# Kernel tuning notes

Hardware: AMD Instinct MI355X
Metric: run time of the kernel (lower is better)

Reference implementation:

```python
import jax, jax.numpy as jnp
import numpy as np

NC = 65536   # candidate centers across FPN levels (single image)
NP = 1024    # proposal boxes == points
D = 256      # points_feat_dim
C = 256      # in_channels (query/key dim)
START_LEVEL = 3
NEG = -1e30


def setup_inputs() -> dict:
    key = jax.random.key(0)
    ks = jax.random.split(key, 9)
    # centers: [y, x, size, stride]; stride in {8,16,32,64,128} -> lvl 0..4
    lvl = jax.random.randint(ks[0], (NC,), 0, 5)
    stride = (2.0 ** (lvl + START_LEVEL)).astype(jnp.float32)
    yx = jax.random.uniform(ks[1], (NC, 2), minval=0.0, maxval=1024.0)
    centers = jnp.concatenate([yx, stride[:, None], stride[:, None]], axis=1)
    # boxes: [x1, y1, x2, y2]
    x1y1 = jax.random.uniform(ks[2], (NP, 2), minval=0.0, maxval=900.0)
    wh = jax.random.uniform(ks[3], (NP, 2), minval=64.0, maxval=256.0)
    boxes = jnp.concatenate([x1y1, x1y1 + wh], axis=1)
    points_feat = jax.random.normal(ks[4], (NP, D), dtype=jnp.float32)
    box_feat = jax.random.normal(ks[5], (NC, D), dtype=jnp.float32)
    Wq = jax.random.normal(ks[6], (D, C), dtype=jnp.float32) / np.sqrt(D).astype(np.float32)
    bq = jnp.zeros((C,), dtype=jnp.float32)
    Wk = jax.random.normal(ks[7], (D, C), dtype=jnp.float32) / np.sqrt(D).astype(np.float32)
    bk = jnp.zeros((C,), dtype=jnp.float32)
    scales = 1.0 + 0.1 * jax.random.normal(ks[8], (5,), dtype=jnp.float32)
    return dict(points_feat=points_feat, box_feat=box_feat, centers=centers,
                boxes=boxes, Wq=Wq, bq=bq, Wk=Wk, bk=bk, scales=scales)


def reference(points_feat, box_feat, centers, boxes, Wq, bq, Wk, bk, scales):
    # geometry -> containment mask [NC, NP] (center c inside box p)
    coord = centers[:, :2] + jnp.floor_divide(centers[:, 2:3], 2.0)  # [NC,2]
    ys, xs = coord[:, 0], coord[:, 1]
    l = xs[:, None] - boxes[None, :, 0]
    t = ys[:, None] - boxes[None, :, 1]
    r = boxes[None, :, 2] - xs[:, None]
    b = boxes[None, :, 3] - ys[:, None]
    mask = jnp.minimum(jnp.minimum(l, t), jnp.minimum(r, b)) > 0     # [NC,NP]

    stride = centers[:, 3]
    lvl = (jnp.log2(stride) - START_LEVEL).astype(jnp.int32)         # [NC] in 0..4
    w = scales[lvl]                                                  # per-level scale

    query = points_feat @ Wq + bq                                    # [NP,C]
    keyf = (box_feat * w[:, None]) @ Wk + bk                         # [NC,C]

    sim = jnp.clip(keyf @ query.T, -50.0, 50.0)                      # [NC,NP]
    logits = jnp.where(mask, sim, NEG)
    attn = jax.nn.softmax(logits, axis=0)
    attn = jnp.where(mask, attn, 0.0)                                # zero out invalid
    merge = attn.T @ box_feat                                        # [NP,D]
    return points_feat + merge
```

## Files before the change

kernel.cpp:

```cpp
#include <hip/hip_runtime.h>

typedef unsigned short ushort_t;
typedef _Float16 half8 __attribute__((ext_vector_type(8)));
typedef short short8 __attribute__((ext_vector_type(8)));
typedef float floatx4 __attribute__((ext_vector_type(4)));

#define NCC 65536
#define NPP 1024
#define DD 256
#define NCHUNK 64
#define VROW 36
#define VTILE_B (256 * VROW * 2)
#define L2E 1.44269504f
#define CLIPL 72.134752f

static __device__ __forceinline__ ushort_t f2h_bits(float x) {
  _Float16 h = (_Float16)x;
  return __builtin_bit_cast(ushort_t, h);
}
static __device__ __forceinline__ ushort_t f2bf_bits(float x) {
  unsigned u = __builtin_bit_cast(unsigned, x);
  unsigned r = (u + 0x7FFFu + ((u >> 16) & 1u)) >> 16;
  return (ushort_t)r;
}
static __device__ __forceinline__ float bf2f(ushort_t b) {
  unsigned u = ((unsigned)b) << 16;
  return __builtin_bit_cast(float, u);
}
static __device__ __forceinline__ half8 cvt8(const float* p) {
  float4 a = *(const float4*)p, b = *(const float4*)(p + 4);
  half8 h;
  h[0] = (_Float16)a.x; h[1] = (_Float16)a.y; h[2] = (_Float16)a.z; h[3] = (_Float16)a.w;
  h[4] = (_Float16)b.x; h[5] = (_Float16)b.y; h[6] = (_Float16)b.z; h[7] = (_Float16)b.w;
  return h;
}
static __device__ __forceinline__ void dma16(const void* g, void* l) {
  __builtin_amdgcn_global_load_lds((const __attribute__((address_space(1))) unsigned int*)g,
                                   (__attribute__((address_space(3))) unsigned int*)l, 16, 0, 0);
}
static __device__ __forceinline__ short8 mk_s8(uint2 lo, uint2 hi) {
  uint4 u;
  u.x = lo.x; u.y = lo.y; u.z = hi.x; u.w = hi.y;
  return __builtin_bit_cast(short8, u);
}

__global__ __launch_bounds__(256) void mk_prep(const float* __restrict__ Wq,
                                               const float* __restrict__ Wk,
                                               const float* __restrict__ bq,
                                               const float* __restrict__ bk,
                                               ushort_t* __restrict__ Mk, float* __restrict__ tu,
                                               float* __restrict__ tv, float* __restrict__ s0v) {
  const int t = threadIdx.x;
  if (blockIdx.x == 16) {
    float su = 0.f, sv = 0.f;
    for (int j = 0; j < DD; j += 4) {
      float4 a = *(const float4*)&Wk[(size_t)t * DD + j];
      float4 b = *(const float4*)&bq[j];
      su += a.x * b.x + a.y * b.y + a.z * b.z + a.w * b.w;
      float4 c = *(const float4*)&Wq[(size_t)t * DD + j];
      float4 d = *(const float4*)&bk[j];
      sv += c.x * d.x + c.y * d.y + c.z * d.z + c.w * d.w;
    }
    tu[t] = su;
    tv[t] = sv;
    __shared__ float red[256];
    red[t] = bk[t] * bq[t];
    __syncthreads();
    for (int o = 128; o; o >>= 1) {
      if (t < o) red[t] += red[t + o];
      __syncthreads();
    }
    if (t == 0) s0v[0] = red[0];
    return;
  }
  const int m0 = ((int)blockIdx.x & 3) * 64, e0 = ((int)blockIdx.x >> 2) * 64;
  const int w = t >> 6, lane = t & 63, qd = lane >> 4, n = lane & 15;
  floatx4 acc[4] = {};
#pragma unroll
  for (int s = 0; s < 8; s++) {
    half8 af = cvt8(&Wk[(size_t)(m0 + w * 16 + n) * DD + s * 32 + qd * 8]);
#pragma unroll
    for (int nt = 0; nt < 4; ++nt) {
      half8 bf = cvt8(&Wq[(size_t)(e0 + nt * 16 + n) * DD + s * 32 + qd * 8]);
      acc[nt] = __builtin_amdgcn_mfma_f32_16x16x32_f16(af, bf, acc[nt], 0, 0, 0);
    }
  }
#pragma unroll
  for (int nt = 0; nt < 4; ++nt)
#pragma unroll
    for (int r = 0; r < 4; r++)
      Mk[(size_t)(m0 + w * 16 + qd * 4 + r) * DD + e0 + nt * 16 + n] = f2h_bits(acc[nt][r]);
}

__global__ __launch_bounds__(256) void gt_prep(const float* __restrict__ pf,
                                               const ushort_t* __restrict__ Mk,
                                               const float* __restrict__ tv,
                                               const float* __restrict__ s0v,
                                               ushort_t* __restrict__ Gt,
                                               float* __restrict__ gamma) {
  const int t = threadIdx.x, p0 = (int)blockIdx.x * 64;
  const int w = t >> 6, lane = t & 63, qd = lane >> 4, n = lane & 15;
  floatx4 acc[16] = {};
#pragma unroll
  for (int s = 0; s < 8; s++) {
    half8 af = cvt8(&pf[(size_t)(p0 + w * 16 + n) * DD + s * 32 + qd * 8]);
#pragma unroll
    for (int nt = 0; nt < 16; ++nt) {
      half8 bf = __builtin_bit_cast(half8,
                                    *(const uint4*)&Mk[(size_t)(nt * 16 + n) * DD + s * 32 + qd * 8]);
      acc[nt] = __builtin_amdgcn_mfma_f32_16x16x32_f16(af, bf, acc[nt], 0, 0, 0);
    }
  }
#pragma unroll
  for (int nt = 0; nt < 16; ++nt)
#pragma unroll
    for (int r = 0; r < 4; r++)
      Gt[(size_t)(p0 + w * 16 + qd * 4 + r) * DD + nt * 16 + n] = f2h_bits(acc[nt][r]);
  if (t < 64) {
    float s = s0v[0];
    for (int j = 0; j < DD; j += 4) {
      float4 a = *(const float4*)&pf[(size_t)(p0 + t) * DD + j];
      float4 b = *(const float4*)&tv[j];
      s += a.x * b.x + a.y * b.y + a.z * b.z + a.w * b.w;
    }
    gamma[p0 + t] = s * L2E - CLIPL;
  }
}

__global__ __launch_bounds__(256) void bt_prep(const float* __restrict__ bf,
                                               const float* __restrict__ centers,
                                               const float* __restrict__ scales,
                                               const float* __restrict__ tu,
                                               ushort_t* __restrict__ bfR,
                                               ushort_t* __restrict__ vTb,
                                               float4* __restrict__ meta) {
  __shared__ float tu_s[256];
  __shared__ __align__(16) ushort_t lt[256][40];
  const int t = threadIdx.x, c0 = (int)blockIdx.x * 32;
  tu_s[t] = tu[t];
  __syncthreads();
  const int c = t >> 3, sub = t & 7;
  float du = 0.f;
#pragma unroll
  for (int i = 0; i < 8; i++) {
    int f4 = sub + 8 * i;
    int d0 = f4 * 4;
    float4 v = *(const float4*)&bf[(size_t)(c0 + c) * DD + d0];
    du += v.x * tu_s[d0] + v.y * tu_s[d0 + 1] + v.z * tu_s[d0 + 2] + v.w * tu_s[d0 + 3];
    int l = f4 >> 1;
    int u = (l & ~7) | ((l & 7) ^ (c & 7));
    ushort_t h0 = f2h_bits(v.x), h1 = f2h_bits(v.y), h2 = f2h_bits(v.z), h3 = f2h_bits(v.w);
    *(uint2*)&bfR[(size_t)(c0 + c) * DD + u * 8 + (d0 & 7)] =
        make_uint2((unsigned)h0 | ((unsigned)h1 << 16), (unsigned)h2 | ((unsigned)h3 << 16));
    lt[d0 + 0][c] = f2bf_bits(v.x);
    lt[d0 + 1][c] = f2bf_bits(v.y);
    lt[d0 + 2][c] = f2bf_bits(v.z);
    lt[d0 + 3][c] = f2bf_bits(v.w);
  }
  du += __shfl_xor(du, 1, 64);
  du += __shfl_xor(du, 2, 64);
  du += __shfl_xor(du, 4, 64);
  if (sub == 0) {
    const float4 ce = *(const float4*)&centers[(size_t)(c0 + c) * 4];
    int lvl = (int)(log2f(ce.w) + 0.5f) - 3;
    lvl = lvl < 0 ? 0 : (lvl > 4 ? 4 : lvl);
    float wsc = scales[lvl];
    float hf = floorf(ce.z * 0.5f);
    meta[c0 + c] = make_float4(wsc * L2E, wsc * du * L2E, ce.y + hf, ce.x + hf);
  }
  __syncthreads();
  char* dst = (char*)vTb + (size_t)blockIdx.x * VTILE_B + (size_t)t * (VROW * 2);
  const char* src = (const char*)&lt[t][0];
#pragma unroll
  for (int i = 0; i < 9; i++) *(uint2*)(dst + i * 8) = *(const uint2*)(src + i * 8);
}

template <bool PART>
__global__ __launch_bounds__(256, 2) void attn_kernel(
    const ushort_t* __restrict__ Gt, const float* __restrict__ gamma,
    const ushort_t* __restrict__ bfR, const ushort_t* __restrict__ vTb,
    const float4* __restrict__ meta, const float* __restrict__ boxes,
    void* __restrict__ acc_out, float* __restrict__ den_out) {
  __shared__ __align__(16) ushort_t lds_k[2][32 * 256];
  __shared__ __align__(16) ushort_t lds_v[2][256 * VROW];
  __shared__ __align__(16) ushort_t lds_p[4][32][VROW];
  __shared__ __align__(16) float4 lds_m[2][32];

  const int t = threadIdx.x;
  const int w = t >> 6, lane = t & 63, qd = lane >> 4, n = lane & 15;
  const int chunk = blockIdx.x;
  const int p0w = blockIdx.y * 128 + w * 32;
  const int cchunk = chunk * 1024;
  const int sw16 = (n & 7) * 16;

  half8 gfr[2][8];
  float4 bxv[2];
  float gam[2];
#pragma unroll
  for (int pt = 0; pt < 2; ++pt) {
    int p = p0w + pt * 16 + n;
#pragma unroll
    for (int s = 0; s < 8; s++)
      gfr[pt][s] = __builtin_bit_cast(half8, *(const uint4*)&Gt[(size_t)p * DD + s * 32 + qd * 8]);
    bxv[pt] = *(const float4*)&boxes[(size_t)p * 4];
    gam[pt] = gamma[p];
  }

  floatx4 macc[2][16] = {};
  float dsum0 = 0.f, dsum1 = 0.f;

  auto stage = [&](int it2, int b) {
    const char* ks = (const char*)bfR + (size_t)(cchunk + it2 * 32) * 512;
    char* kd = (char*)lds_k[b];
#pragma unroll
    for (int j = 0; j < 4; ++j) {
      int i = w * 4 + j;
      dma16(ks + i * 1024 + lane * 16, kd + i * 1024 + lane * 16);
    }
    const char* vs = (const char*)vTb + ((size_t)(cchunk >> 5) + it2) * VTILE_B;
    char* vd = (char*)lds_v[b];
#pragma unroll
    for (int j = 0; j < 4; ++j) {
      int i = j * 4 + w;
      dma16(vs + i * 1024 + lane * 16, vd + i * 1024 + lane * 16);
    }
    if (w < 2) {
      int i = 16 + w;
      dma16(vs + i * 1024 + lane * 16, vd + i * 1024 + lane * 16);
    }
    if (w == 0 && lane < 32)
      dma16((const char*)meta + (size_t)(cchunk + it2 * 32) * 16 + lane * 16,
            (char*)lds_m[b] + lane * 16);
  };

  stage(0, 0);

  for (int it = 0; it < 32; ++it) {
    const int buf = it & 1;
    __syncthreads();
    if (it + 1 < 32) stage(it + 1, buf ^ 1);

#pragma unroll
    for (int t2 = 0; t2 < 2; ++t2) {
      const char* krow = (const char*)lds_k[buf] + (t2 * 16 + n) * 512;
      floatx4 a0 = {}, a1 = {};
#pragma unroll
      for (int s = 0; s < 8; s++) {
        half8 af = __builtin_bit_cast(half8, *(const uint4*)(krow + ((s * 64 + qd * 16) ^ sw16)));
        a0 = __builtin_amdgcn_mfma_f32_16x16x32_f16(af, gfr[0][s], a0, 0, 0, 0);
        a1 = __builtin_amdgcn_mfma_f32_16x16x32_f16(af, gfr[1][s], a1, 0, 0, 0);
      }
      unsigned pk00 = 0, pk01 = 0, pk10 = 0, pk11 = 0;
#pragma unroll
      for (int r = 0; r < 4; r++) {
        int cl = t2 * 16 + qd * 4 + r;
        float4 mt = lds_m[buf][cl];
        {
          float mn = fminf(fminf(mt.z - bxv[0].x, mt.w - bxv[0].y),
                           fminf(bxv[0].z - mt.z, bxv[0].w - mt.w));
          float targ = fmaf(mt.x, a0[r], mt.y) + gam[0];
          float e = (mn > 0.f) ? exp2f(fminf(targ, 0.f)) : 0.f;
          dsum0 += e;
          unsigned b = (unsigned)f2bf_bits(e);
          if (r == 0) pk00 = b;
          else if (r == 1) pk00 |= b << 16;
          else if (r == 2) pk01 = b;
          else pk01 |= b << 16;
        }
        {
          float mn = fminf(fminf(mt.z - bxv[1].x, mt.w - bxv[1].y),
                           fminf(bxv[1].z - mt.z, bxv[1].w - mt.w));
          float targ = fmaf(mt.x, a1[r], mt.y) + gam[1];
          float e = (mn > 0.f) ? exp2f(fminf(targ, 0.f)) : 0.f;
          dsum1 += e;
          unsigned b = (unsigned)f2bf_bits(e);
          if (r == 0) pk10 = b;
          else if (r == 1) pk10 |= b << 16;
          else if (r == 2) pk11 = b;
          else pk11 |= b << 16;
        }
      }
      *(uint2*)&lds_p[w][n][t2 * 16 + qd * 4] = make_uint2(pk00, pk01);
      *(uint2*)&lds_p[w][16 + n][t2 * 16 + qd * 4] = make_uint2(pk10, pk11);
    }
    __asm__ volatile("s_waitcnt lgkmcnt(0)" ::: "memory");

    const char* pr0 = (const char*)&lds_p[w][n][0];
    const char* pr1 = (const char*)&lds_p[w][16 + n][0];
    short8 a20 = mk_s8(*(const uint2*)(pr0 + qd * 16), *(const uint2*)(pr0 + qd * 16 + 8));
    short8 a21 = mk_s8(*(const uint2*)(pr1 + qd * 16), *(const uint2*)(pr1 + qd * 16 + 8));
#pragma unroll
    for (int dt = 0; dt < 16; ++dt) {
      const char* vrow = (const char*)lds_v[buf] + (dt * 16 + n) * (VROW * 2);
      short8 b2 = mk_s8(*(const uint2*)(vrow + qd * 16), *(const uint2*)(vrow + qd * 16 + 8));
      macc[0][dt] = __builtin_amdgcn_mfma_f32_16x16x32_bf16(a20, b2, macc[0][dt], 0, 0, 0);
      macc[1][dt] = __builtin_amdgcn_mfma_f32_16x16x32_bf16(a21, b2, macc[1][dt], 0, 0, 0);
    }
  }

  dsum0 += __shfl_xor(dsum0, 16, 64);
  dsum0 += __shfl_xor(dsum0, 32, 64);
  dsum1 += __shfl_xor(dsum1, 16, 64);
  dsum1 += __shfl_xor(dsum1, 32, 64);

  if (PART) {
    if (lane < 16) {
      den_out[(size_t)chunk * NPP + p0w + n] = dsum0;
      den_out[(size_t)chunk * NPP + p0w + 16 + n] = dsum1;
    }
    ushort_t* ab = (ushort_t*)acc_out + (size_t)chunk * NPP * DD;
#pragma unroll
    for (int pt = 0; pt < 2; ++pt)
#pragma unroll
      for (int dt = 0; dt < 16; ++dt)
#pragma unroll
        for (int r = 0; r < 4; r++)
          ab[(size_t)(p0w + pt * 16 + qd * 4 + r) * DD + dt * 16 + n] = f2bf_bits(macc[pt][dt][r]);
  } else {
    if (lane < 16) {
      atomicAdd(&den_out[p0w + n], dsum0);
      atomicAdd(&den_out[p0w + 16 + n], dsum1);
    }
    float* ab = (float*)acc_out;
#pragma unroll
    for (int pt = 0; pt < 2; ++pt)
#pragma unroll
      for (int dt = 0; dt < 16; ++dt)
#pragma unroll
        for (int r = 0; r < 4; r++)
          atomicAdd(&ab[(size_t)(p0w + pt * 16 + qd * 4 + r) * DD + dt * 16 + n],
                    macc[pt][dt][r]);
  }
}

__global__ __launch_bounds__(256) void reduce_finalize(const float* __restrict__ points_feat,
                                                       const ushort_t* __restrict__ acc_part,
                                                       const float* __restrict__ den_part,
                                                       float* __restrict__ out) {
  const int p = blockIdx.x, t = threadIdx.x;
  float s = 0.f;
#pragma unroll 4
  for (int c = 0; c < NCHUNK; ++c) s += bf2f(acc_part[((size_t)c * NPP + p) * DD + t]);
  float dn = den_part[(size_t)(t & 63) * NPP + p];
#pragma unroll
  for (int o = 1; o < 64; o <<= 1) dn += __shfl_xor(dn, o, 64);
  float m = (dn > 0.f) ? s / dn : 0.f;
  out[(size_t)p * DD + t] = points_feat[(size_t)p * DD + t] + m;
}

__global__ void finalize(const float* __restrict__ points_feat, const float* __restrict__ acc,
                         const float* __restrict__ den, float* __restrict__ out) {
  int p = blockIdx.x, d = threadIdx.x;
  float dn = den[p];
  float m = (dn > 0.f) ? acc[p * DD + d] / dn : 0.f;
  out[p * DD + d] = points_feat[p * DD + d] + m;
}

extern "C" void kernel_launch(void* const* d_in, const int* in_sizes, int n_in, void* d_out,
                              int out_size, void* d_ws, size_t ws_size, hipStream_t stream) {
  const float* points_feat = (const float*)d_in[0];
  const float* box_feat = (const float*)d_in[1];
  const float* centers = (const float*)d_in[2];
  const float* boxes = (const float*)d_in[3];
  const float* Wq = (const float*)d_in[4];
  const float* bq = (const float*)d_in[5];
  const float* Wk = (const float*)d_in[6];
  const float* bk = (const float*)d_in[7];
  const float* scales = (const float*)d_in[8];

  char* p = (char*)d_ws;
  ushort_t* ws_accP = (ushort_t*)p;  p += (size_t)NCHUNK * NPP * DD * 2;
  float* ws_den = (float*)p;         p += (size_t)NCHUNK * NPP * 4;
  ushort_t* ws_bfR = (ushort_t*)p;   p += (size_t)NCC * DD * 2;
  ushort_t* ws_vTb = (ushort_t*)p;   p += (size_t)(NCC / 32) * VTILE_B;
  ushort_t* ws_Gt = (ushort_t*)p;    p += (size_t)NPP * DD * 2;
  float4* ws_meta = (float4*)p;      p += (size_t)NCC * 16;
  float* ws_gamma = (float*)p;       p += (size_t)NPP * 4;
  size_t need_part = (size_t)(p - (char*)d_ws);

  if (ws_size >= need_part) {
    ushort_t* ws_Mk = ws_accP;
    float* ws_tu = (float*)(ws_Mk + (size_t)DD * DD);
    float* ws_tv = ws_tu + DD;
    float* ws_s0 = ws_tv + DD;

    mk_prep<<<17, 256, 0, stream>>>(Wq, Wk, bq, bk, ws_Mk, ws_tu, ws_tv, ws_s0);
    gt_prep<<<16, 256, 0, stream>>>(points_feat, ws_Mk, ws_tv, ws_s0, ws_Gt, ws_gamma);
    bt_prep<<<NCC / 32, 256, 0, stream>>>(box_feat, centers, scales, ws_tu, ws_bfR, ws_vTb,
                                          ws_meta);
    attn_kernel<true><<<dim3(NCHUNK, 8), 256, 0, stream>>>(ws_Gt, ws_gamma, ws_bfR, ws_vTb,
                                                           ws_meta, boxes, ws_accP, ws_den);
    reduce_finalize<<<NPP, 256, 0, stream>>>(points_feat, ws_accP, ws_den, (float*)d_out);
  } else {
    char* q = (char*)d_ws;
    ushort_t* f_bfR = (ushort_t*)q;  q += (size_t)NCC * DD * 2;
    ushort_t* f_vTb = (ushort_t*)q;  q += (size_t)(NCC / 32) * VTILE_B;
    ushort_t* f_Gt = (ushort_t*)q;   q += (size_t)NPP * DD * 2;
    float4* f_meta = (float4*)q;     q += (size_t)NCC * 16;
    float* f_gamma = (float*)q;      q += (size_t)NPP * 4;
    float* f_den = (float*)q;        q += (size_t)NPP * 4;
    float* f_acc = (float*)q;        q += (size_t)NPP * DD * 4;
    ushort_t* f_Mk = (ushort_t*)f_acc;
    float* f_tu = (float*)(f_Mk + (size_t)DD * DD);
    float* f_tv = f_tu + DD;
    float* f_s0 = f_tv + DD;

    mk_prep<<<17, 256, 0, stream>>>(Wq, Wk, bq, bk, f_Mk, f_tu, f_tv, f_s0);
    gt_prep<<<16, 256, 0, stream>>>(points_feat, f_Mk, f_tv, f_s0, f_Gt, f_gamma);
    bt_prep<<<NCC / 32, 256, 0, stream>>>(box_feat, centers, scales, f_tu, f_bfR, f_vTb, f_meta);
    hipMemsetAsync(f_den, 0, ((size_t)NPP * DD + NPP) * sizeof(float), stream);
    attn_kernel<false><<<dim3(NCHUNK, 8), 256, 0, stream>>>(f_Gt, f_gamma, f_bfR, f_vTb, f_meta,
                                                            boxes, f_acc, f_den);
    finalize<<<NPP, DD, 0, stream>>>(points_feat, f_acc, f_den, (float*)d_out);
  }
}
```

Measured before the change: 299.3 us.

## Keep softmax probabilities in registers via permuted key rows and fuse prep kernels

The attention kernel now reads QK tiles in a permuted row order so the bf16 probabilities land directly in the MFMA A-operand layout, removing the LDS round trip for P. Meta is read straight from global memory instead of being staged through LDS. The bfR swizzle key is changed to match the new row order. The V tile row is padded to 40 for 16-byte vector loads. The Gt and bt prep kernels are merged into one launch, with Mk written in a fragment-friendly layout. This trades LDS traffic, waits and one launch for more global meta loads and a larger V tile in LDS.

```diff
diff --git a/kernel.cpp b/kernel.cpp
--- a/kernel.cpp
+++ b/kernel.cpp
@@ -9,7 +9,7 @@
 #define NPP 1024
 #define DD 256
 #define NCHUNK 64
-#define VROW 36
+#define VROW 40
 #define VTILE_B (256 * VROW * 2)
 #define L2E 1.44269504f
 #define CLIPL 72.134752f
@@ -38,17 +38,12 @@
   __builtin_amdgcn_global_load_lds((const __attribute__((address_space(1))) unsigned int*)g,
                                    (__attribute__((address_space(3))) unsigned int*)l, 16, 0, 0);
 }
-static __device__ __forceinline__ short8 mk_s8(uint2 lo, uint2 hi) {
-  uint4 u;
-  u.x = lo.x; u.y = lo.y; u.z = hi.x; u.w = hi.y;
-  return __builtin_bit_cast(short8, u);
-}
 
 __global__ __launch_bounds__(256) void mk_prep(const float* __restrict__ Wq,
                                                const float* __restrict__ Wk,
                                                const float* __restrict__ bq,
                                                const float* __restrict__ bk,
-                                               ushort_t* __restrict__ Mk, float* __restrict__ tu,
+                                               ushort_t* __restrict__ MkF, float* __restrict__ tu,
                                                float* __restrict__ tv, float* __restrict__ s0v) {
   const int t = threadIdx.x;
   if (blockIdx.x == 16) {
@@ -88,58 +83,59 @@
 #pragma unroll
   for (int nt = 0; nt < 4; ++nt)
 #pragma unroll
-    for (int r = 0; r < 4; r++)
-      Mk[(size_t)(m0 + w * 16 + qd * 4 + r) * DD + e0 + nt * 16 + n] = f2h_bits(acc[nt][r]);
-}
-
-__global__ __launch_bounds__(256) void gt_prep(const float* __restrict__ pf,
-                                               const ushort_t* __restrict__ Mk,
-                                               const float* __restrict__ tv,
-                                               const float* __restrict__ s0v,
-                                               ushort_t* __restrict__ Gt,
-                                               float* __restrict__ gamma) {
-  const int t = threadIdx.x, p0 = (int)blockIdx.x * 64;
-  const int w = t >> 6, lane = t & 63, qd = lane >> 4, n = lane & 15;
-  floatx4 acc[16] = {};
-#pragma unroll
-  for (int s = 0; s < 8; s++) {
-    half8 af = cvt8(&pf[(size_t)(p0 + w * 16 + n) * DD + s * 32 + qd * 8]);
-#pragma unroll
-    for (int nt = 0; nt < 16; ++nt) {
-      half8 bf = __builtin_bit_cast(half8,
-                                    *(const uint4*)&Mk[(size_t)(nt * 16 + n) * DD + s * 32 + qd * 8]);
-      acc[nt] = __builtin_amdgcn_mfma_f32_16x16x32_f16(af, bf, acc[nt], 0, 0, 0);
-    }
-  }
-#pragma unroll
-  for (int nt = 0; nt < 16; ++nt)
-#pragma unroll
-    for (int r = 0; r < 4; r++)
-      Gt[(size_t)(p0 + w * 16 + qd * 4 + r) * DD + nt * 16 + n] = f2h_bits(acc[nt][r]);
-  if (t < 64) {
-    float s = s0v[0];
-    for (int j = 0; j < DD; j += 4) {
-      float4 a = *(const float4*)&pf[(size_t)(p0 + t) * DD + j];
-      float4 b = *(const float4*)&tv[j];
-      s += a.x * b.x + a.y * b.y + a.z * b.z + a.w * b.w;
-    }
-    gamma[p0 + t] = s * L2E - CLIPL;
-  }
-}
-
-__global__ __launch_bounds__(256) void bt_prep(const float* __restrict__ bf,
-                                               const float* __restrict__ centers,
-                                               const float* __restrict__ scales,
-                                               const float* __restrict__ tu,
-                                               ushort_t* __restrict__ bfR,
-                                               ushort_t* __restrict__ vTb,
-                                               float4* __restrict__ meta) {
+    for (int r = 0; r < 4; r++) {
+      int mr = m0 + w * 16 + qd * 4 + r;
+      int e = e0 + nt * 16 + n;
+      size_t slot = ((size_t)(mr >> 4) * 8 + (e >> 5)) * 64 + ((e >> 3) & 3) * 16 + (mr & 15);
+      MkF[slot * 8 + (e & 7)] = f2h_bits(acc[nt][r]);
+    }
+}
+
+__global__ __launch_bounds__(256) void btgt_prep(
+    const float* __restrict__ bf, const float* __restrict__ pf,
+    const float* __restrict__ centers, const float* __restrict__ scales,
+    const float* __restrict__ tu, const float* __restrict__ tv,
+    const float* __restrict__ s0v, const ushort_t* __restrict__ MkF,
+    ushort_t* __restrict__ bfR, ushort_t* __restrict__ vTb, float4* __restrict__ meta,
+    ushort_t* __restrict__ Gt, float* __restrict__ gamma) {
+  const int t = threadIdx.x;
+  if (blockIdx.x >= (NCC / 32)) {
+    const int p0 = ((int)blockIdx.x - NCC / 32) * 64;
+    const int w = t >> 6, lane = t & 63, qd = lane >> 4, n = lane & 15;
+    floatx4 acc[16] = {};
+#pragma unroll
+    for (int s = 0; s < 8; s++) {
+      half8 af = cvt8(&pf[(size_t)(p0 + w * 16 + n) * DD + s * 32 + qd * 8]);
+#pragma unroll
+      for (int nt = 0; nt < 16; ++nt) {
+        half8 bfr = __builtin_bit_cast(
+            half8, *(const uint4*)&MkF[(((size_t)nt * 8 + s) * 64 + lane) * 8]);
+        acc[nt] = __builtin_amdgcn_mfma_f32_16x16x32_f16(af, bfr, acc[nt], 0, 0, 0);
+      }
+    }
+#pragma unroll
+    for (int nt = 0; nt < 16; ++nt)
+#pragma unroll
+      for (int r = 0; r < 4; r++)
+        Gt[(size_t)(p0 + w * 16 + qd * 4 + r) * DD + nt * 16 + n] = f2h_bits(acc[nt][r]);
+    if (t < 64) {
+      float s = s0v[0];
+      for (int j = 0; j < DD; j += 4) {
+        float4 a = *(const float4*)&pf[(size_t)(p0 + t) * DD + j];
+        float4 b = *(const float4*)&tv[j];
+        s += a.x * b.x + a.y * b.y + a.z * b.z + a.w * b.w;
+      }
+      gamma[p0 + t] = s * L2E - CLIPL;
+    }
+    return;
+  }
   __shared__ float tu_s[256];
-  __shared__ __align__(16) ushort_t lt[256][40];
-  const int t = threadIdx.x, c0 = (int)blockIdx.x * 32;
+  __shared__ __align__(16) ushort_t lt[256][VROW];
+  const int c0 = (int)blockIdx.x * 32;
   tu_s[t] = tu[t];
   __syncthreads();
   const int c = t >> 3, sub = t & 7;
+  const int kc = ((c0 + c) & 3) | (((c0 + c) >> 1) & 4);
   float du = 0.f;
 #pragma unroll
   for (int i = 0; i < 8; i++) {
@@ -148,7 +144,7 @@
     float4 v = *(const float4*)&bf[(size_t)(c0 + c) * DD + d0];
     du += v.x * tu_s[d0] + v.y * tu_s[d0 + 1] + v.z * tu_s[d0 + 2] + v.w * tu_s[d0 + 3];
     int l = f4 >> 1;
-    int u = (l & ~7) | ((l & 7) ^ (c & 7));
+    int u = (l & ~7) | ((l & 7) ^ kc);
     ushort_t h0 = f2h_bits(v.x), h1 = f2h_bits(v.y), h2 = f2h_bits(v.z), h3 = f2h_bits(v.w);
     *(uint2*)&bfR[(size_t)(c0 + c) * DD + u * 8 + (d0 & 7)] =
         make_uint2((unsigned)h0 | ((unsigned)h1 << 16), (unsigned)h2 | ((unsigned)h3 << 16));
@@ -172,7 +168,7 @@
   char* dst = (char*)vTb + (size_t)blockIdx.x * VTILE_B + (size_t)t * (VROW * 2);
   const char* src = (const char*)&lt[t][0];
 #pragma unroll
-  for (int i = 0; i < 9; i++) *(uint2*)(dst + i * 8) = *(const uint2*)(src + i * 8);
+  for (int i = 0; i < 5; i++) *(uint4*)(dst + i * 16) = *(const uint4*)(src + i * 16);
 }
 
 template <bool PART>
@@ -183,8 +179,6 @@
     void* __restrict__ acc_out, float* __restrict__ den_out) {
   __shared__ __align__(16) ushort_t lds_k[2][32 * 256];
   __shared__ __align__(16) ushort_t lds_v[2][256 * VROW];
-  __shared__ __align__(16) ushort_t lds_p[4][32][VROW];
-  __shared__ __align__(16) float4 lds_m[2][32];
 
   const int t = threadIdx.x;
   const int w = t >> 6, lane = t & 63, qd = lane >> 4, n = lane & 15;
@@ -220,79 +214,71 @@
     const char* vs = (const char*)vTb + ((size_t)(cchunk >> 5) + it2) * VTILE_B;
     char* vd = (char*)lds_v[b];
 #pragma unroll
-    for (int j = 0; j < 4; ++j) {
-      int i = j * 4 + w;
+    for (int j = 0; j < 5; ++j) {
+      int i = w * 5 + j;
       dma16(vs + i * 1024 + lane * 16, vd + i * 1024 + lane * 16);
     }
-    if (w < 2) {
-      int i = 16 + w;
-      dma16(vs + i * 1024 + lane * 16, vd + i * 1024 + lane * 16);
-    }
-    if (w == 0 && lane < 32)
-      dma16((const char*)meta + (size_t)(cchunk + it2 * 32) * 16 + lane * 16,
-            (char*)lds_m[b] + lane * 16);
   };
 
   stage(0, 0);
 
   for (int it = 0; it < 32; ++it) {
     const int buf = it & 1;
+    const int cb = cchunk + it * 32;
     __syncthreads();
     if (it + 1 < 32) stage(it + 1, buf ^ 1);
 
+    floatx4 at[2][2] = {};
 #pragma unroll
     for (int t2 = 0; t2 < 2; ++t2) {
-      const char* krow = (const char*)lds_k[buf] + (t2 * 16 + n) * 512;
-      floatx4 a0 = {}, a1 = {};
+      const char* krow =
+          (const char*)lds_k[buf] + ((((n & 12) << 1) + (n & 3) + 4 * t2) * 512);
 #pragma unroll
       for (int s = 0; s < 8; s++) {
         half8 af = __builtin_bit_cast(half8, *(const uint4*)(krow + ((s * 64 + qd * 16) ^ sw16)));
-        a0 = __builtin_amdgcn_mfma_f32_16x16x32_f16(af, gfr[0][s], a0, 0, 0, 0);
-        a1 = __builtin_amdgcn_mfma_f32_16x16x32_f16(af, gfr[1][s], a1, 0, 0, 0);
+        at[t2][0] = __builtin_amdgcn_mfma_f32_16x16x32_f16(af, gfr[0][s], at[t2][0], 0, 0, 0);
+        at[t2][1] = __builtin_amdgcn_mfma_f32_16x16x32_f16(af, gfr[1][s], at[t2][1], 0, 0, 0);
       }
-      unsigned pk00 = 0, pk01 = 0, pk10 = 0, pk11 = 0;
+    }
+    unsigned pk0[4], pk1[4];
+#pragma unroll
+    for (int t2 = 0; t2 < 2; ++t2) {
 #pragma unroll
       for (int r = 0; r < 4; r++) {
-        int cl = t2 * 16 + qd * 4 + r;
-        float4 mt = lds_m[buf][cl];
+        float4 mt = meta[cb + 8 * qd + 4 * t2 + r];
         {
           float mn = fminf(fminf(mt.z - bxv[0].x, mt.w - bxv[0].y),
                            fminf(bxv[0].z - mt.z, bxv[0].w - mt.w));
-          float targ = fmaf(mt.x, a0[r], mt.y) + gam[0];
+          float targ = fmaf(mt.x, at[t2][0][r], mt.y) + gam[0];
           float e = (mn > 0.f) ? exp2f(fminf(targ, 0.f)) : 0.f;
           dsum0 += e;
           unsigned b = (unsigned)f2bf_bits(e);
-          if (r == 0) pk00 = b;
-          else if (r == 1) pk00 |= b << 16;
-          else if (r == 2) pk01 = b;
-          else pk01 |= b << 16;
+          unsigned idx = t2 * 2 + (r >> 1);
+          if ((r & 1) == 0) pk0[idx] = b;
+          else pk0[idx] |= b << 16;
         }
         {
           float mn = fminf(fminf(mt.z - bxv[1].x, mt.w - bxv[1].y),
                            fminf(bxv[1].z - mt.z, bxv[1].w - mt.w));
-          float targ = fmaf(mt.x, a1[r], mt.y) + gam[1];
+          float targ = fmaf(mt.x, at[t2][1][r], mt.y) + gam[1];
           float e = (mn > 0.f) ? exp2f(fminf(targ, 0.f)) : 0.f;
           dsum1 += e;
           unsigned b = (unsigned)f2bf_bits(e);
-          if (r == 0) pk10 = b;
-          else if (r == 1) pk10 |= b << 16;
-          else if (r == 2) pk11 = b;
-          else pk11 |= b << 16;
+          unsigned idx = t2 * 2 + (r >> 1);
+          if ((r & 1) == 0) pk1[idx] = b;
+          else pk1[idx] |= b << 16;
         }
       }
-      *(uint2*)&lds_p[w][n][t2 * 16 + qd * 4] = make_uint2(pk00, pk01);
-      *(uint2*)&lds_p[w][16 + n][t2 * 16 + qd * 4] = make_uint2(pk10, pk11);
-    }
-    __asm__ volatile("s_waitcnt lgkmcnt(0)" ::: "memory");
-
-    const char* pr0 = (const char*)&lds_p[w][n][0];
-    const char* pr1 = (const char*)&lds_p[w][16 + n][0];
-    short8 a20 = mk_s8(*(const uint2*)(pr0 + qd * 16), *(const uint2*)(pr0 + qd * 16 + 8));
-    short8 a21 = mk_s8(*(const uint2*)(pr1 + qd * 16), *(const uint2*)(pr1 + qd * 16 + 8));
+    }
+    uint4 u0, u1;
+    u0.x = pk0[0]; u0.y = pk0[1]; u0.z = pk0[2]; u0.w = pk0[3];
+    u1.x = pk1[0]; u1.y = pk1[1]; u1.z = pk1[2]; u1.w = pk1[3];
+    short8 a20 = __builtin_bit_cast(short8, u0);
+    short8 a21 = __builtin_bit_cast(short8, u1);
 #pragma unroll
     for (int dt = 0; dt < 16; ++dt) {
-      const char* vrow = (const char*)lds_v[buf] + (dt * 16 + n) * (VROW * 2);
-      short8 b2 = mk_s8(*(const uint2*)(vrow + qd * 16), *(const uint2*)(vrow + qd * 16 + 8));
+      short8 b2 = __builtin_bit_cast(
+          short8, *(const uint4*)&lds_v[buf][(dt * 16 + n) * VROW + qd * 8]);
       macc[0][dt] = __builtin_amdgcn_mfma_f32_16x16x32_bf16(a20, b2, macc[0][dt], 0, 0, 0);
       macc[1][dt] = __builtin_amdgcn_mfma_f32_16x16x32_bf16(a21, b2, macc[1][dt], 0, 0, 0);
     }
@@ -385,9 +371,9 @@
     float* ws_s0 = ws_tv + DD;
 
     mk_prep<<<17, 256, 0, stream>>>(Wq, Wk, bq, bk, ws_Mk, ws_tu, ws_tv, ws_s0);
-    gt_prep<<<16, 256, 0, stream>>>(points_feat, ws_Mk, ws_tv, ws_s0, ws_Gt, ws_gamma);
-    bt_prep<<<NCC / 32, 256, 0, stream>>>(box_feat, centers, scales, ws_tu, ws_bfR, ws_vTb,
-                                          ws_meta);
+    btgt_prep<<<NCC / 32 + 16, 256, 0, stream>>>(box_feat, points_feat, centers, scales, ws_tu,
+                                                 ws_tv, ws_s0, ws_Mk, ws_bfR, ws_vTb, ws_meta,
+                                                 ws_Gt, ws_gamma);
     attn_kernel<true><<<dim3(NCHUNK, 8), 256, 0, stream>>>(ws_Gt, ws_gamma, ws_bfR, ws_vTb,
                                                            ws_meta, boxes, ws_accP, ws_den);
     reduce_finalize<<<NPP, 256, 0, stream>>>(points_feat, ws_accP, ws_den, (float*)d_out);
@@ -406,8 +392,9 @@
     float* f_s0 = f_tv + DD;
 
     mk_prep<<<17, 256, 0, stream>>>(Wq, Wk, bq, bk, f_Mk, f_tu, f_tv, f_s0);
-    gt_prep<<<16, 256, 0, stream>>>(points_feat, f_Mk, f_tv, f_s0, f_Gt, f_gamma);
-    bt_prep<<<NCC / 32, 256, 0, stream>>>(box_feat, centers, scales, f_tu, f_bfR, f_vTb, f_meta);
+    btgt_prep<<<NCC / 32 + 16, 256, 0, stream>>>(box_feat, points_feat, centers, scales, f_tu,
+                                                 f_tv, f_s0, f_Mk, f_bfR, f_vTb, f_meta, f_Gt,
+                                                 f_gamma);
     hipMemsetAsync(f_den, 0, ((size_t)NPP * DD + NPP) * sizeof(float), stream);
     attn_kernel<false><<<dim3(NCHUNK, 8), 256, 0, stream>>>(f_Gt, f_gamma, f_bfR, f_vTb, f_meta,
                                                             boxes, f_acc, f_den);
```

Measured after the change: 307.4 us. +2.7%, slower.
